# Optimization experiments

Measured on AMD Instinct MI355X. Metric: run time of the kernel, lower is better.

## Reference

```python
import jax, jax.numpy as jnp
import numpy as np

MARGIN = 1.0
EPS = 1e-16


def setup_inputs() -> dict:
    key = jax.random.key(0)
    k1, k2 = jax.random.split(key)
    B, E = 512, 128
    embs = jax.random.normal(k1, (B, E), dtype=jnp.float32)
    labels = jax.random.randint(k2, (B,), 0, 64, dtype=jnp.int64)
    return {"embs": embs, "labels": labels}


def _triplet_mask(labels):
    # [B,B,B] mask: valid (a,p,n) iff a!=p, a!=n, p!=n, label[a]==label[p], label[a]!=label[n]
    B = labels.shape[0]
    neq = ~jnp.eye(B, dtype=bool)
    idx_mask = neq[:, :, None] & neq[:, None, :] & neq[None, :, :]
    lab_eq = labels[:, None] == labels[None, :]
    lab_mask = lab_eq[:, :, None] & (~lab_eq)[:, None, :]
    return idx_mask & lab_mask


def reference(embs, labels):
    # pairwise squared L2 distances (squared=True path, no sqrt)
    dot = embs @ embs.T                      # [B,B]
    sq_norm = jnp.diagonal(dot)              # [B]
    dist = sq_norm[:, None] - 2.0 * dot + sq_norm[None, :]
    dist = jnp.maximum(dist, 0.0)            # [B,B]

    # triplet losses: d(a,p) - d(a,n) + margin, over [B,B,B]
    triplet_loss = dist[:, :, None] - dist[:, None, :] + MARGIN
    mask = _triplet_mask(labels)
    triplet_loss = jnp.maximum(triplet_loss * mask.astype(triplet_loss.dtype), 0.0)

    n_pos = jnp.sum(triplet_loss > EPS)
    return jnp.sum(triplet_loss) / (n_pos.astype(triplet_loss.dtype) + EPS)
```

## Files before the change

kernel.cpp:

```cpp
#include <hip/hip_runtime.h>
#include <hip/hip_bf16.h>


#define BSZ 512
#define EDIM 128
#define TS 32
#define NPOSMAX 96

typedef __attribute__((ext_vector_type(8))) short short8;
typedef __attribute__((ext_vector_type(4))) float f32x4;

__device__ __forceinline__ unsigned short f2bf(float f) {
    __hip_bfloat16 h = __float2bfloat16(f);
    return *reinterpret_cast<unsigned short*>(&h);
}

__global__ __launch_bounds__(256) void dist_mfma_sym(
    const float* __restrict__ embs,
    float* __restrict__ D)
{
    __shared__ unsigned short Abf[TS][136];
    __shared__ unsigned short Bbf[TS][136];
    __shared__ float nA[TS], nB[TS];

    const int tid = threadIdx.x;

    int t = blockIdx.x, bi = 0;
    while (t >= 16 - bi) { t -= 16 - bi; ++bi; }
    const int bj = bi + t;
    const int I = bi * TS, J = bj * TS;
    const int wv = tid >> 6, lane = tid & 63;

    const float4* E4 = reinterpret_cast<const float4*>(embs);

#pragma unroll
    for (int q = 0; q < 4; ++q) {
        int idx = tid + 256 * q;
        int r   = idx >> 5;
        int k4  = idx & 31;

        float4 va = E4[(size_t)(I + r) * (EDIM / 4) + k4];
        float sa = va.x * va.x + va.y * va.y + va.z * va.z + va.w * va.w;
        sa += __shfl_xor(sa, 1); sa += __shfl_xor(sa, 2); sa += __shfl_xor(sa, 4);
        sa += __shfl_xor(sa, 8); sa += __shfl_xor(sa, 16);
        if ((tid & 31) == 0) nA[r] = sa;
        ushort4 ua = { f2bf(va.x), f2bf(va.y), f2bf(va.z), f2bf(va.w) };
        *reinterpret_cast<ushort4*>(&Abf[r][k4 * 4]) = ua;

        float4 vb = E4[(size_t)(J + r) * (EDIM / 4) + k4];
        float sb = vb.x * vb.x + vb.y * vb.y + vb.z * vb.z + vb.w * vb.w;
        sb += __shfl_xor(sb, 1); sb += __shfl_xor(sb, 2); sb += __shfl_xor(sb, 4);
        sb += __shfl_xor(sb, 8); sb += __shfl_xor(sb, 16);
        if ((tid & 31) == 0) nB[r] = sb;
        ushort4 ub = { f2bf(-2.f * vb.x), f2bf(-2.f * vb.y),
                       f2bf(-2.f * vb.z), f2bf(-2.f * vb.w) };
        *reinterpret_cast<ushort4*>(&Bbf[r][k4 * 4]) = ub;
    }
    __syncthreads();

    const int qi = wv >> 1, qj = wv & 1;
    const int l15 = lane & 15, lk = lane >> 4;

    f32x4 acc;
#pragma unroll
    for (int reg = 0; reg < 4; ++reg)
        acc[reg] = nA[qi * 16 + lk * 4 + reg] + nB[qj * 16 + l15];

    const unsigned short* arow = &Abf[qi * 16 + l15][0];
    const unsigned short* brow = &Bbf[qj * 16 + l15][0];
#pragma unroll
    for (int ks = 0; ks < 4; ++ks) {
        short8 af = *reinterpret_cast<const short8*>(arow + ks * 32 + lk * 8);
        short8 bf = *reinterpret_cast<const short8*>(brow + ks * 32 + lk * 8);
        acc = __builtin_amdgcn_mfma_f32_16x16x32_bf16(af, bf, acc, 0, 0, 0);
    }

#pragma unroll
    for (int reg = 0; reg < 4; ++reg) acc[reg] = fmaxf(acc[reg], 0.f);

#pragma unroll
    for (int reg = 0; reg < 4; ++reg) {
        int row = I + qi * 16 + lk * 4 + reg;
        int col = J + qj * 16 + l15;
        D[(size_t)row * BSZ + col] = acc[reg];
    }

    if (bi != bj) {
        int mrow = J + qj * 16 + l15;
        int mcol = I + qi * 16 + lk * 4;
        float4 m = make_float4(acc[0], acc[1], acc[2], acc[3]);
        *reinterpret_cast<float4*>(&D[(size_t)mrow * BSZ + mcol]) = m;
    }
}

__global__ __launch_bounds__(256) void triplet_pass(
    const float* __restrict__ D,
    const int* __restrict__ labels,
    float* __restrict__ sums,
    float* __restrict__ cnts)
{
    __shared__ int   lab[BSZ];
    __shared__ float d[BSZ];
    __shared__ unsigned long long masks[8];
    __shared__ int   plist[NPOSMAX];
    __shared__ float wsum[4];
    __shared__ int   wcnt[4];

    const int a = blockIdx.x, tid = threadIdx.x;
    const int wv = tid >> 6, lane = tid & 63;

    lab[tid]       = labels[tid];
    lab[tid + 256] = labels[tid + 256];
    float2 dv = reinterpret_cast<const float2*>(D + (size_t)a * BSZ)[tid];
    d[tid * 2]     = dv.x;
    d[tid * 2 + 1] = dv.y;
    __syncthreads();

    const int la = lab[a];

#pragma unroll
    for (int c = 0; c < 2; ++c) {
        int j = c * 256 + tid;
        unsigned long long m = __ballot(lab[j] == la && j != a);
        if (lane == 0) masks[c * 4 + wv] = m;
    }
    __syncthreads();

    int np = 0;
#pragma unroll
    for (int m = 0; m < 8; ++m) np += __popcll(masks[m]);
    if (np > NPOSMAX) np = NPOSMAX;

#pragma unroll
    for (int c = 0; c < 2; ++c) {
        int j = c * 256 + tid;
        if (lab[j] == la && j != a) {
            int mi = c * 4 + wv, off = 0;
            for (int m = 0; m < mi; ++m) off += __popcll(masks[m]);
            off += __popcll(masks[mi] & ((1ull << lane) - 1ull));
            if (off < NPOSMAX) plist[off] = j;
        }
    }
    __syncthreads();

    float s = 0.f;
    int   cnt = 0;
#pragma unroll
    for (int c = 0; c < 2; ++c) {
        int n = c * 256 + tid;
        if (lab[n] != la) {
            float dn = d[n];
            for (int i = 0; i < np; ++i) {
                float t = fmaxf(d[plist[i]] - dn + 1.0f, 0.f);
                s += t;
                cnt += (t > 1e-16f) ? 1 : 0;
            }
        }
    }

#pragma unroll
    for (int off = 32; off; off >>= 1) {
        s   += __shfl_down(s, off);
        cnt += __shfl_down(cnt, off);
    }
    if (lane == 0) { wsum[wv] = s; wcnt[wv] = cnt; }
    __syncthreads();
    if (tid == 0) {
        sums[a] = wsum[0] + wsum[1] + wsum[2] + wsum[3];
        cnts[a] = (float)(wcnt[0] + wcnt[1] + wcnt[2] + wcnt[3]);
    }
}

__global__ __launch_bounds__(512) void finalize(
    const float* __restrict__ sums,
    const float* __restrict__ cnts,
    float* __restrict__ out)
{
    __shared__ float wsum[8], wcnt[8];
    const int tid = threadIdx.x;
    float s = sums[tid];
    float c = cnts[tid];
#pragma unroll
    for (int off = 32; off; off >>= 1) {
        s += __shfl_down(s, off);
        c += __shfl_down(c, off);
    }
    const int wv = tid >> 6, lane = tid & 63;
    if (lane == 0) { wsum[wv] = s; wcnt[wv] = c; }
    __syncthreads();
    if (tid == 0) {
        float S = 0.f, C = 0.f;
#pragma unroll
        for (int w = 0; w < 8; ++w) { S += wsum[w]; C += wcnt[w]; }
        out[0] = S / (C + 1e-16f);
    }
}

extern "C" void kernel_launch(void* const* d_in, const int* in_sizes, int n_in,
                              void* d_out, int out_size, void* d_ws, size_t ws_size,
                              hipStream_t stream)
{
    const float* embs   = reinterpret_cast<const float*>(d_in[0]);
    const int*   labels = reinterpret_cast<const int*>(d_in[1]);
    float*       out    = reinterpret_cast<float*>(d_out);

    float* D    = reinterpret_cast<float*>(d_ws);
    float* sums = D + (size_t)BSZ * BSZ;
    float* cnts = sums + BSZ;

    dist_mfma_sym<<<136, 256, 0, stream>>>(embs, D);
    triplet_pass<<<BSZ, 256, 0, stream>>>(D, labels, sums, cnts);
    finalize<<<1, 512, 0, stream>>>(sums, cnts, out);
}
```

Before: 15.65 us.

## Fuse final reduction into triplet pass via fixed-point atomics and last-block detection

```diff
diff --git a/kernel.cpp b/kernel.cpp
--- a/kernel.cpp
+++ b/kernel.cpp
@@ -6,6 +6,8 @@
 #define EDIM 128
 #define TS 32
 #define NPOSMAX 96
+#define FPSCALE 1048576.0
+#define ARRSHIFT 54
 
 typedef __attribute__((ext_vector_type(8))) short short8;
 typedef __attribute__((ext_vector_type(4))) float f32x4;
@@ -17,13 +19,15 @@
 
 __global__ __launch_bounds__(256) void dist_mfma_sym(
     const float* __restrict__ embs,
-    float* __restrict__ D)
+    float* __restrict__ D,
+    unsigned long long* __restrict__ accs)
 {
     __shared__ unsigned short Abf[TS][136];
     __shared__ unsigned short Bbf[TS][136];
     __shared__ float nA[TS], nB[TS];
 
     const int tid = threadIdx.x;
+    if (blockIdx.x == 0 && tid < 2) accs[tid] = 0ull;
 
     int t = blockIdx.x, bi = 0;
     while (t >= 16 - bi) { t -= 16 - bi; ++bi; }
@@ -96,8 +100,8 @@
 __global__ __launch_bounds__(256) void triplet_pass(
     const float* __restrict__ D,
     const int* __restrict__ labels,
-    float* __restrict__ sums,
-    float* __restrict__ cnts)
+    unsigned long long* __restrict__ accs,
+    float* __restrict__ out)
 {
     __shared__ int   lab[BSZ];
     __shared__ float d[BSZ];
@@ -165,34 +169,21 @@
     }
     if (lane == 0) { wsum[wv] = s; wcnt[wv] = cnt; }
     __syncthreads();
+
     if (tid == 0) {
-        sums[a] = wsum[0] + wsum[1] + wsum[2] + wsum[3];
-        cnts[a] = (float)(wcnt[0] + wcnt[1] + wcnt[2] + wcnt[3]);
-    }
-}
-
-__global__ __launch_bounds__(512) void finalize(
-    const float* __restrict__ sums,
-    const float* __restrict__ cnts,
-    float* __restrict__ out)
-{
-    __shared__ float wsum[8], wcnt[8];
-    const int tid = threadIdx.x;
-    float s = sums[tid];
-    float c = cnts[tid];
-#pragma unroll
-    for (int off = 32; off; off >>= 1) {
-        s += __shfl_down(s, off);
-        c += __shfl_down(c, off);
-    }
-    const int wv = tid >> 6, lane = tid & 63;
-    if (lane == 0) { wsum[wv] = s; wcnt[wv] = c; }
-    __syncthreads();
-    if (tid == 0) {
-        float S = 0.f, C = 0.f;
-#pragma unroll
-        for (int w = 0; w < 8; ++w) { S += wsum[w]; C += wcnt[w]; }
-        out[0] = S / (C + 1e-16f);
+        float Sb = wsum[0] + wsum[1] + wsum[2] + wsum[3];
+        unsigned long long qs = (unsigned long long)llrint((double)Sb * FPSCALE);
+        unsigned long long qc = (unsigned long long)(wcnt[0] + wcnt[1] + wcnt[2] + wcnt[3]);
+
+        atomicAdd(&accs[1], qc);
+        asm volatile("s_waitcnt vmcnt(0)" ::: "memory");
+        unsigned long long old =
+            atomicAdd(&accs[0], qs | (1ull << ARRSHIFT));
+        if ((old >> ARRSHIFT) == (unsigned long long)(BSZ - 1)) {
+            unsigned long long S = (old & ((1ull << ARRSHIFT) - 1ull)) + qs;
+            unsigned long long C = atomicAdd(&accs[1], 0ull);
+            out[0] = (float)(((double)S / FPSCALE) / ((double)C + 1e-16));
+        }
     }
 }
 
@@ -204,11 +195,10 @@
     const int*   labels = reinterpret_cast<const int*>(d_in[1]);
     float*       out    = reinterpret_cast<float*>(d_out);
 
-    float* D    = reinterpret_cast<float*>(d_ws);
-    float* sums = D + (size_t)BSZ * BSZ;
-    float* cnts = sums + BSZ;
-
-    dist_mfma_sym<<<136, 256, 0, stream>>>(embs, D);
-    triplet_pass<<<BSZ, 256, 0, stream>>>(D, labels, sums, cnts);
-    finalize<<<1, 512, 0, stream>>>(sums, cnts, out);
-}
+    float* D = reinterpret_cast<float*>(d_ws);
+    unsigned long long* accs =
+        reinterpret_cast<unsigned long long*>(D + (size_t)BSZ * BSZ);
+
+    dist_mfma_sym<<<136, 256, 0, stream>>>(embs, D, accs);
+    triplet_pass<<<BSZ, 256, 0, stream>>>(D, labels, accs, out);
+}
```

After: 25.80 us. 64.9% more time.
